# Performance work log

Hardware: AMD Instinct MI355X
Metric: run time of the kernel (lower is better)

## Reference

```python
import jax, jax.numpy as jnp
import numpy as np

B, S, H, NH, HD = 4, 2048, 2048, 16, 128
SCALE = HD ** -0.5


def rotate_half(x):
    x1, x2 = jnp.split(x, 2, axis=-1)
    return jnp.concatenate([-x2, x1], axis=-1)


def setup_inputs() -> dict:
    key = jax.random.key(0)
    ks = jax.random.split(key, 8)
    x = jax.random.normal(ks[0], (B, S, H), dtype=jnp.float32)
    # RoPE tables for positions 0..S-1, standard theta=10000 construction
    inv_freq = 1.0 / (10000.0 ** (jnp.arange(0, HD, 2, dtype=jnp.float32) / HD))
    t = jnp.arange(S, dtype=jnp.float32)
    freqs = jnp.einsum('s,d->sd', t, inv_freq)          # [S, HD/2]
    emb = jnp.concatenate([freqs, freqs], axis=-1)      # [S, HD]
    cos, sin = jnp.cos(emb), jnp.sin(emb)
    # causal mask: True = masked (future positions)
    mask = jnp.triu(jnp.ones((S, S), dtype=bool), k=1)
    std = H ** -0.5
    Wq = jax.random.normal(ks[1], (H, H), dtype=jnp.float32) * std
    Wk = jax.random.normal(ks[2], (H, H), dtype=jnp.float32) * std
    Wv = jax.random.normal(ks[3], (H, H), dtype=jnp.float32) * std
    Wo = jax.random.normal(ks[4], (H, H), dtype=jnp.float32) * std
    return {"x": x, "cos": cos, "sin": sin, "mask": mask,
            "Wq": Wq, "Wk": Wk, "Wv": Wv, "Wo": Wo}


def reference(x, cos, sin, mask, Wq, Wk, Wv, Wo):
    # projections: nn.Linear(bias=False) => x @ W.T
    def proj(W):
        y = jnp.einsum('bsh,ih->bsi', x, W)             # [B,S,inner]
        return y.reshape(B, S, NH, HD).transpose(0, 2, 1, 3)  # [B,NH,S,HD]
    q, k, v = proj(Wq), proj(Wk), proj(Wv)
    # RoPE (rotate-half), cos/sin broadcast over batch & heads
    c = cos[None, None, :, :]
    s = sin[None, None, :, :]
    q = q * c + rotate_half(q) * s
    k = k * c + rotate_half(k) * s
    # attention
    attn = jnp.einsum('bhqd,bhkd->bhqk', q, k) * SCALE
    attn = jnp.where(mask[None, None, :, :], -jnp.inf, attn)
    attn = jax.nn.softmax(attn, axis=-1)
    out = jnp.einsum('bhqk,bhkd->bhqd', attn, v)
    out = out.transpose(0, 2, 1, 3).reshape(B, S, NH * HD)
    y = jnp.einsum('bsi,hi->bsh', out, Wo)
    return y, k, v
```

## Files before the change

### kernel.cpp

```cpp
#include <hip/hip_runtime.h>
#include <hip/hip_bf16.h>
#include <math.h>

typedef __bf16 bf16_t;
typedef __bf16 bf16x8 __attribute__((ext_vector_type(8)));
typedef __bf16 bf16x4v __attribute__((ext_vector_type(4)));
typedef float  f32x4  __attribute__((ext_vector_type(4)));
typedef float  f32x16 __attribute__((ext_vector_type(16)));
typedef unsigned int u32x4 __attribute__((ext_vector_type(4)));

constexpr int CB = 4, CS = 2048, CH = 2048, CNH = 16, CHD = 128;
constexpr int CM = CB * CS;
constexpr float CSCALE = 0.08838834764831845f;
constexpr float CL2E   = 1.4426950408889634f;
constexpr float CSC2   = CSCALE * CL2E;

__device__ __forceinline__ float fexp2(float x) {
  float r;
  asm("v_exp_f32 %0, %1" : "=v"(r) : "v"(x));
  return r;
}

__device__ __forceinline__ void g2l16(const void* g, void* l) {
  __builtin_amdgcn_global_load_lds(
      (const __attribute__((address_space(1))) void*)g,
      (__attribute__((address_space(3))) void*)l, 16, 0, 0);
}

__global__ __launch_bounds__(256) void cvt_kernel(const float* __restrict__ in,
                                                  bf16_t* __restrict__ out, int n4) {
  int i = blockIdx.x * 256 + threadIdx.x;
  if (i >= n4) return;
  float4 v = reinterpret_cast<const float4*>(in)[i];
  bf16x4v o = {(bf16_t)v.x, (bf16_t)v.y, (bf16_t)v.z, (bf16_t)v.w};
  reinterpret_cast<bf16x4v*>(out)[i] = o;
}

__device__ __forceinline__ void gemm256sq_core(const bf16_t* __restrict__ A,
                                               const bf16_t* __restrict__ Bm,
                                               bf16_t (*As2)[4][64 * 64],
                                               bf16_t (*Bs2)[4][64 * 64],
                                               int row0, int col0,
                                               f32x4 (&acc)[8][4]) {
  const int tid = threadIdx.x, lane = tid & 63, w = tid >> 6;
  const int wm = w >> 2, wn = w & 3;
  constexpr int NKT = CH / 64;
  const int id = w * 64 + lane;
  const int rl = id >> 3, ck = id & 7;

  auto stA = [&](int buf, int kt, int q) {
    const int row = q * 64 + rl;
    g2l16(A + (size_t)(row0 + row) * CH + kt * 64 + ((ck ^ (row & 7)) << 3),
          &As2[buf][q][id * 8]);
  };
  auto stB = [&](int buf, int kt, int q) {
    const int row = q * 64 + rl;
    g2l16(Bm + (size_t)(col0 + row) * CH + kt * 64 + ((ck ^ (row & 7)) << 3),
          &Bs2[buf][q][id * 8]);
  };
  auto rdA = [&](int buf, int r, int c) -> bf16x8 {
    return *(const bf16x8*)(&As2[buf][r >> 6][(r & 63) * 64 + ((c ^ (r & 7)) << 3)]);
  };
  auto rdB = [&](int buf, int r, int c) -> bf16x8 {
    return *(const bf16x8*)(&Bs2[buf][r >> 6][(r & 63) * 64 + ((c ^ (r & 7)) << 3)]);
  };

#pragma unroll
  for (int q = 0; q < 4; ++q) stB(0, 0, q);
#pragma unroll
  for (int q = 0; q < 4; ++q) stA(0, 0, q);
  asm volatile("s_waitcnt vmcnt(0)" ::: "memory");
  __builtin_amdgcn_s_barrier();
  __builtin_amdgcn_sched_barrier(0);

  const int ar0 = wm * 128 + (lane & 15);
  const int br0 = wn * 64 + (lane & 15);
  const int chi = lane >> 4;

  for (int t = 0; t < NKT; ++t) {
    const int buf = t & 1, nbuf = buf ^ 1;
    const bool pf = (t + 1 < NKT);
    bf16x8 bb[4][2], aa[2][2];

#pragma unroll
    for (int p = 0; p < 4; ++p) {
      if (p == 0) {
#pragma unroll
        for (int nf = 0; nf < 4; ++nf)
#pragma unroll
          for (int kk = 0; kk < 2; ++kk)
            bb[nf][kk] = rdB(buf, br0 + nf * 16, kk * 4 + chi);
      }
#pragma unroll
      for (int i = 0; i < 2; ++i)
#pragma unroll
        for (int kk = 0; kk < 2; ++kk)
          aa[i][kk] = rdA(buf, ar0 + (2 * p + i) * 16, kk * 4 + chi);

      if (pf) {
        if (p == 0) { stB(nbuf, t + 1, 0); stB(nbuf, t + 1, 1); }
        if (p == 1) { stB(nbuf, t + 1, 2); stB(nbuf, t + 1, 3); }
        if (p == 2) { stA(nbuf, t + 1, 0); stA(nbuf, t + 1, 2); }
        if (p == 3) { stA(nbuf, t + 1, 1); stA(nbuf, t + 1, 3); }
      }

      __builtin_amdgcn_s_barrier();
      asm volatile("s_waitcnt lgkmcnt(0)" ::: "memory");
      __builtin_amdgcn_sched_barrier(0);
      __builtin_amdgcn_s_setprio(1);
#pragma unroll
      for (int i = 0; i < 2; ++i)
#pragma unroll
        for (int nf = 0; nf < 4; ++nf)
#pragma unroll
          for (int kk = 0; kk < 2; ++kk)
            acc[2 * p + i][nf] = __builtin_amdgcn_mfma_f32_16x16x32_bf16(
                aa[i][kk], bb[nf][kk], acc[2 * p + i][nf], 0, 0, 0);
      __builtin_amdgcn_s_setprio(0);

      if (p == 1) {
        if (pf) { asm volatile("s_waitcnt vmcnt(4)" ::: "memory"); }
        else    { asm volatile("s_waitcnt vmcnt(0)" ::: "memory"); }
      }
      if (p == 3 && pf) { asm volatile("s_waitcnt vmcnt(2)" ::: "memory"); }
      __builtin_amdgcn_s_barrier();
      __builtin_amdgcn_sched_barrier(0);
    }
  }
}

__global__ __launch_bounds__(512, 1) void qkv_gemm(const bf16_t* __restrict__ xb,
                                                   const bf16_t* __restrict__ wqb,
                                                   const bf16_t* __restrict__ wkb,
                                                   const bf16_t* __restrict__ wvb,
                                                   bf16_t* __restrict__ qraw,
                                                   bf16_t* __restrict__ knat,
                                                   bf16_t* __restrict__ vt2,
                                                   float* __restrict__ vout) {
  __shared__ __align__(16) bf16_t As2[2][4][64 * 64];
  __shared__ __align__(16) bf16_t Bs2[2][4][64 * 64];
  const int z = blockIdx.z;
  const bf16_t* Bm = (z == 0) ? wqb : ((z == 1) ? wkb : wvb);
  const int row0 = blockIdx.x * 256, col0 = blockIdx.y * 256;
  f32x4 acc[8][4] = {};
  gemm256sq_core(xb, Bm, As2, Bs2, row0, col0, acc);

  const int lane = threadIdx.x & 63, w = threadIdx.x >> 6;
  const int wm = w >> 2, wn = w & 3;
#pragma unroll
  for (int i = 0; i < 8; ++i) {
#pragma unroll
    for (int j = 0; j < 4; ++j) {
      const int gr0 = row0 + wm * 128 + i * 16 + (lane >> 4) * 4;
      const int gc = col0 + wn * 64 + j * 16 + (lane & 15);
      const int b = gr0 >> 11, s0 = gr0 & (CS - 1);
      const int nh = gc >> 7, hd = gc & (CHD - 1);
      const int bh = b * CNH + nh;
      if (z == 2) {
#pragma unroll
        for (int r = 0; r < 4; ++r) {
          const size_t idx = ((size_t)bh * CS + s0 + r) * CHD + hd;
          vout[idx] = acc[i][j][r];
        }
        bf16x4v pv = {(bf16_t)acc[i][j][0], (bf16_t)acc[i][j][1],
                      (bf16_t)acc[i][j][2], (bf16_t)acc[i][j][3]};
        *(bf16x4v*)(vt2 + (((size_t)bh * (CS / 16) + (s0 >> 4)) * CHD + hd) * 16 +
                    (s0 & 15)) = pv;
      } else if (z == 1) {
        bf16_t* kp = knat + (((size_t)bh * 8 + (hd >> 4)) * CS + s0) * 16 + (hd & 15);
#pragma unroll
        for (int r = 0; r < 4; ++r) kp[r * 16] = (bf16_t)acc[i][j][r];
      } else {
#pragma unroll
        for (int r = 0; r < 4; ++r) {
          const size_t idx = ((size_t)bh * CS + s0 + r) * CHD + hd;
          qraw[idx] = (bf16_t)acc[i][j][r];
        }
      }
    }
  }
}

__global__ __launch_bounds__(512, 1) void y_gemm(const bf16_t* __restrict__ ob,
                                                 const bf16_t* __restrict__ wob,
                                                 float* __restrict__ yout) {
  __shared__ __align__(16) bf16_t As2[2][4][64 * 64];
  __shared__ __align__(16) bf16_t Bs2[2][4][64 * 64];
  const int row0 = blockIdx.x * 256, col0 = blockIdx.y * 256;
  f32x4 acc[8][4] = {};
  gemm256sq_core(ob, wob, As2, Bs2, row0, col0, acc);
  const int lane = threadIdx.x & 63, w = threadIdx.x >> 6;
  const int wm = w >> 2, wn = w & 3;
#pragma unroll
  for (int i = 0; i < 8; ++i)
#pragma unroll
    for (int j = 0; j < 4; ++j)
#pragma unroll
      for (int r = 0; r < 4; ++r) {
        const int gr = row0 + wm * 128 + i * 16 + (lane >> 4) * 4 + r;
        const int gc = col0 + wn * 64 + j * 16 + (lane & 15);
        yout[(size_t)gr * CH + gc] = acc[i][j][r];
      }
}

__global__ __launch_bounds__(256) void rope_kernel(bf16_t* __restrict__ qraw,
                                                   bf16_t* __restrict__ knat,
                                                   const float* __restrict__ cosd,
                                                   const float* __restrict__ sind,
                                                   float* __restrict__ kout) {
  const int gid = blockIdx.x * 256 + threadIdx.x;
  if (blockIdx.y == 0) {
    bf16_t* p = qraw;
    const int row = gid >> 3, d0 = (gid & 7) << 3;
    const int s = row & (CS - 1);
    const size_t base = (size_t)row * CHD;
    bf16x8 v1 = *(bf16x8*)(p + base + d0);
    bf16x8 v2 = *(bf16x8*)(p + base + d0 + 64);
    float c[8], sn[8];
    *(float4*)(c)      = *(const float4*)(cosd + s * CHD + d0);
    *(float4*)(c + 4)  = *(const float4*)(cosd + s * CHD + d0 + 4);
    *(float4*)(sn)     = *(const float4*)(sind + s * CHD + d0);
    *(float4*)(sn + 4) = *(const float4*)(sind + s * CHD + d0 + 4);
    bf16x8 o1, o2;
#pragma unroll
    for (int i = 0; i < 8; ++i) {
      const float x1 = (float)v1[i], x2 = (float)v2[i];
      o1[i] = (bf16_t)(x1 * c[i] - x2 * sn[i]);
      o2[i] = (bf16_t)(x2 * c[i] + x1 * sn[i]);
    }
    *(bf16x8*)(p + base + d0) = o1;
    *(bf16x8*)(p + base + d0 + 64) = o2;
  } else {
    const int row = gid >> 3, sub = gid & 7;
    const int pan = sub >> 1, hf = (sub & 1) * 8;
    const int bh = row >> 11, s = row & (CS - 1);
    const int d0 = pan * 16 + hf;
    bf16_t* k1 = knat + (((size_t)bh * 8 + pan) * CS + s) * 16 + hf;
    bf16_t* k2 = knat + (((size_t)bh * 8 + pan + 4) * CS + s) * 16 + hf;
    bf16x8 v1 = *(bf16x8*)k1;
    bf16x8 v2 = *(bf16x8*)k2;
    float c[8], sn[8];
    *(float4*)(c)      = *(const float4*)(cosd + s * CHD + d0);
    *(float4*)(c + 4)  = *(const float4*)(cosd + s * CHD + d0 + 4);
    *(float4*)(sn)     = *(const float4*)(sind + s * CHD + d0);
    *(float4*)(sn + 4) = *(const float4*)(sind + s * CHD + d0 + 4);
    float f1[8], f2[8];
    bf16x8 o1, o2;
#pragma unroll
    for (int i = 0; i < 8; ++i) {
      const float x1 = (float)v1[i], x2 = (float)v2[i];
      f1[i] = x1 * c[i] - x2 * sn[i];
      f2[i] = x2 * c[i] + x1 * sn[i];
      o1[i] = (bf16_t)f1[i];
      o2[i] = (bf16_t)f2[i];
    }
    *(bf16x8*)k1 = o1;
    *(bf16x8*)k2 = o2;
    const size_t kb = (size_t)row * CHD + d0;
    *(float4*)(kout + kb)          = *(float4*)(f1);
    *(float4*)(kout + kb + 4)      = *(float4*)(f1 + 4);
    *(float4*)(kout + kb + 64)     = *(float4*)(f2);
    *(float4*)(kout + kb + 64 + 4) = *(float4*)(f2 + 4);
  }
}

__global__ __launch_bounds__(128) void attn_kernel(const bf16_t* __restrict__ qb,
                                                   const bf16_t* __restrict__ kn,
                                                   const bf16_t* __restrict__ v2,
                                                   bf16_t* __restrict__ ob) {
  const int tid = threadIdx.x, lane = tid & 63, w = tid >> 6;
  const int hi = lane >> 5, l31 = lane & 31;

  const int swz = (blockIdx.x & 7) * 256 + (blockIdx.x >> 3);
  const int bh = swz >> 5;
  const int qt = (31 - (swz & 31)) * 2 + w;

  const int b = bh >> 4, nh = bh & (CNH - 1);
  const bf16_t* kbase = kn + (size_t)bh * 8 * CS * 16;
  const bf16_t* vbase = v2 + (size_t)bh * (CS / 16) * CHD * 16;
  const int qw0 = qt * 32;
  const int qrow = qw0 + l31;

  bf16x8 bq[8];
  {
    const bf16_t* qp = qb + ((size_t)bh * CS + qrow) * CHD + hi * 8;
#pragma unroll
    for (int ks = 0; ks < 8; ++ks) bq[ks] = *(const bf16x8*)(qp + ks * 16);
  }

  float m_ = -INFINITY, l_ = 0.f;
  f32x16 o_[4] = {};

  const int nt = (qt >> 1) + 1;
  for (int kt = 0; kt < nt; ++kt) {
    const int kvb = kt * 64;

    f32x16 st[2] = {};
#pragma unroll
    for (int kb2 = 0; kb2 < 2; ++kb2) {
      const bf16_t* kr = kbase + (size_t)(kvb + kb2 * 32 + l31) * 16 + hi * 8;
#pragma unroll
      for (int ks = 0; ks < 8; ++ks) {
        bf16x8 ak = *(const bf16x8*)(kr + (size_t)ks * CS * 16);
        st[kb2] = __builtin_amdgcn_mfma_f32_32x32x16_bf16(ak, bq[ks], st[kb2], 0, 0, 0);
      }
    }

    const bool anymask = (kvb + 63) > qw0;
#pragma unroll
    for (int blk = 0; blk < 2; ++blk)
#pragma unroll
      for (int r = 0; r < 16; ++r) {
        float xv = st[blk][r] * CSC2;
        if (anymask) {
          const int kv = kvb + blk * 32 + 4 * hi + (r & 3) + 8 * (r >> 2);
          if (kv > qrow) xv = -INFINITY;
        }
        st[blk][r] = xv;
      }

    float tmax = st[0][0];
#pragma unroll
    for (int r = 1; r < 16; ++r) tmax = fmaxf(tmax, st[0][r]);
#pragma unroll
    for (int r = 0; r < 16; ++r) tmax = fmaxf(tmax, st[1][r]);
    tmax = fmaxf(tmax, __shfl_xor(tmax, 32, 64));

    if (__any(tmax - m_ > 8.0f)) {
      const float mn = fmaxf(m_, tmax);
      const float corr = fexp2(m_ - mn);
      m_ = mn;
      l_ *= corr;
#pragma unroll
      for (int hb = 0; hb < 4; ++hb) o_[hb] *= corr;
    }

    float psum = 0.f;
#pragma unroll
    for (int blk = 0; blk < 2; ++blk)
#pragma unroll
      for (int r = 0; r < 16; ++r) {
        const float pv = fexp2(st[blk][r] - m_);
        st[blk][r] = pv;
        psum += pv;
      }
    psum += __shfl_xor(psum, 32, 64);
    l_ += psum;

    bf16x8 pb[4];
#pragma unroll
    for (int ks = 0; ks < 4; ++ks) {
      const int blk = ks >> 1, r0 = (ks & 1) * 8;
      unsigned pw0, pw1, pw2, pw3;
      asm("v_cvt_pk_bf16_f32 %0, %1, %2" : "=v"(pw0) : "v"(st[blk][r0 + 0]), "v"(st[blk][r0 + 1]));
      asm("v_cvt_pk_bf16_f32 %0, %1, %2" : "=v"(pw2) : "v"(st[blk][r0 + 4]), "v"(st[blk][r0 + 5]));
      asm("v_cvt_pk_bf16_f32 %0, %1, %2" : "=v"(pw1) : "v"(st[blk][r0 + 2]), "v"(st[blk][r0 + 3]));
      asm("v_cvt_pk_bf16_f32 %0, %1, %2" : "=v"(pw3) : "v"(st[blk][r0 + 6]), "v"(st[blk][r0 + 7]));
      asm("v_permlane32_swap_b32 %0, %1" : "+v"(pw0), "+v"(pw2));
      asm("v_permlane32_swap_b32 %0, %1" : "+v"(pw1), "+v"(pw3));
      u32x4 pk = {pw0, pw1, pw2, pw3};
      pb[ks] = *reinterpret_cast<bf16x8*>(&pk);
    }

#pragma unroll
    for (int hb = 0; hb < 4; ++hb) {
      const bf16_t* vr = vbase + ((size_t)(kvb >> 4) * CHD + hb * 32 + l31) * 16 + hi * 8;
#pragma unroll
      for (int ks = 0; ks < 4; ++ks) {
        bf16x8 av = *(const bf16x8*)(vr + (size_t)ks * CHD * 16);
        o_[hb] = __builtin_amdgcn_mfma_f32_32x32x16_bf16(av, pb[ks], o_[hb], 0, 0, 0);
      }
    }
  }

  const float linv = 1.0f / l_;
  bf16_t* orow = ob + ((size_t)(b * CS + qrow)) * CH + nh * CHD;
#pragma unroll
  for (int hb = 0; hb < 4; ++hb)
#pragma unroll
    for (int g = 0; g < 4; ++g) {
      bf16x4v pv = {(bf16_t)(o_[hb][4 * g + 0] * linv), (bf16_t)(o_[hb][4 * g + 1] * linv),
                    (bf16_t)(o_[hb][4 * g + 2] * linv), (bf16_t)(o_[hb][4 * g + 3] * linv)};
      *(bf16x4v*)(orow + hb * 32 + 4 * hi + 8 * g) = pv;
    }
}

extern "C" void kernel_launch(void* const* d_in, const int* in_sizes, int n_in,
                              void* d_out, int out_size, void* d_ws, size_t ws_size,
                              hipStream_t stream) {
  const float* x    = (const float*)d_in[0];
  const float* cosd = (const float*)d_in[1];
  const float* sind = (const float*)d_in[2];
  const float* Wq = (const float*)d_in[4];
  const float* Wk = (const float*)d_in[5];
  const float* Wv = (const float*)d_in[6];
  const float* Wo = (const float*)d_in[7];

  float* yout = (float*)d_out;
  float* kout = yout + (size_t)CM * CH;
  float* vout = kout + (size_t)CM * CH;

  char* ws = (char*)d_ws;
  size_t off = 0;
  auto wsalloc = [&](size_t bytes) {
    void* p = ws + off;
    off += (bytes + 255) & ~(size_t)255;
    return p;
  };
  bf16_t* xb   = (bf16_t*)wsalloc((size_t)CM * CH * 2);
  bf16_t* wqb  = (bf16_t*)wsalloc((size_t)CH * CH * 2);
  bf16_t* wkb  = (bf16_t*)wsalloc((size_t)CH * CH * 2);
  bf16_t* wvb  = (bf16_t*)wsalloc((size_t)CH * CH * 2);
  bf16_t* wob  = (bf16_t*)wsalloc((size_t)CH * CH * 2);
  bf16_t* qraw = (bf16_t*)wsalloc((size_t)CM * CH * 2);
  bf16_t* knat = (bf16_t*)wsalloc((size_t)CM * CH * 2);
  bf16_t* vt2  = (bf16_t*)wsalloc((size_t)CM * CH * 2);
  bf16_t* ob   = (bf16_t*)wsalloc((size_t)CM * CH * 2);

  cvt_kernel<<<CM * CH / 4 / 256, 256, 0, stream>>>(x, xb, CM * CH / 4);
  cvt_kernel<<<CH * CH / 4 / 256, 256, 0, stream>>>(Wq, wqb, CH * CH / 4);
  cvt_kernel<<<CH * CH / 4 / 256, 256, 0, stream>>>(Wk, wkb, CH * CH / 4);
  cvt_kernel<<<CH * CH / 4 / 256, 256, 0, stream>>>(Wv, wvb, CH * CH / 4);
  cvt_kernel<<<CH * CH / 4 / 256, 256, 0, stream>>>(Wo, wob, CH * CH / 4);

  qkv_gemm<<<dim3(CM / 256, CH / 256, 3), 512, 0, stream>>>(xb, wqb, wkb, wvb,
                                                            qraw, knat, vt2, vout);
  rope_kernel<<<dim3(CB * CNH * CS * 8 / 256, 2), 256, 0, stream>>>(qraw, knat, cosd,
                                                                    sind, kout);
  attn_kernel<<<CB * CNH * (CS / 64), 128, 0, stream>>>(qraw, knat, vt2, ob);
  y_gemm<<<dim3(CM / 256, CH / 256), 512, 0, stream>>>(ob, wob, yout);
}
```

Before: 532.3 us.

## Split attention KV loop across two waves per query tile with LDS merge

Each block now handles one 32-row query tile, and its two waves process alternating KV tiles. The second wave writes its partial O, max and sum to shared memory, and the first wave merges them with rescaling before writing the output. Twice as many blocks are launched, which is meant to improve load balance and occupancy across the causal triangle. The cost is an extra LDS round trip, a barrier, and Q loads that are duplicated per wave.

```diff
diff --git a/kernel.cpp b/kernel.cpp
--- a/kernel.cpp
+++ b/kernel.cpp
@@ -268,12 +268,14 @@
                                                    const bf16_t* __restrict__ kn,
                                                    const bf16_t* __restrict__ v2,
                                                    bf16_t* __restrict__ ob) {
-  const int tid = threadIdx.x, lane = tid & 63, w = tid >> 6;
+  __shared__ float Os[32][129];
+  __shared__ float Ms[32], Ls[32];
+  const int tid = threadIdx.x, lane = tid & 63, wh = tid >> 6;
   const int hi = lane >> 5, l31 = lane & 31;
 
-  const int swz = (blockIdx.x & 7) * 256 + (blockIdx.x >> 3);
-  const int bh = swz >> 5;
-  const int qt = (31 - (swz & 31)) * 2 + w;
+  const int swz = (blockIdx.x & 7) * 512 + (blockIdx.x >> 3);
+  const int bh = swz >> 6;
+  const int qt = 63 - (swz & 63);
 
   const int b = bh >> 4, nh = bh & (CNH - 1);
   const bf16_t* kbase = kn + (size_t)bh * 8 * CS * 16;
@@ -292,7 +294,7 @@
   f32x16 o_[4] = {};
 
   const int nt = (qt >> 1) + 1;
-  for (int kt = 0; kt < nt; ++kt) {
+  for (int kt = wh; kt < nt; kt += 2) {
     const int kvb = kt * 64;
 
     f32x16 st[2] = {};
@@ -373,15 +375,35 @@
     }
   }
 
-  const float linv = 1.0f / l_;
+  if (wh == 1) {
+#pragma unroll
+    for (int hb = 0; hb < 4; ++hb)
+#pragma unroll
+      for (int r = 0; r < 16; ++r) {
+        const int hd = 32 * hb + 4 * hi + (r & 3) + 8 * (r >> 2);
+        Os[l31][hd] = o_[hb][r];
+      }
+    if (hi == 0) { Ms[l31] = m_; Ls[l31] = l_; }
+  }
+  __builtin_amdgcn_s_barrier();
+  if (wh == 1) return;
+
+  const float m1 = Ms[l31], l1 = Ls[l31];
+  const float mn = fmaxf(m_, m1);
+  const float c0 = fexp2(m_ - mn), c1 = fexp2(m1 - mn);
+  const float linv = 1.0f / (l_ * c0 + l1 * c1);
   bf16_t* orow = ob + ((size_t)(b * CS + qrow)) * CH + nh * CHD;
 #pragma unroll
   for (int hb = 0; hb < 4; ++hb)
 #pragma unroll
     for (int g = 0; g < 4; ++g) {
-      bf16x4v pv = {(bf16_t)(o_[hb][4 * g + 0] * linv), (bf16_t)(o_[hb][4 * g + 1] * linv),
-                    (bf16_t)(o_[hb][4 * g + 2] * linv), (bf16_t)(o_[hb][4 * g + 3] * linv)};
-      *(bf16x4v*)(orow + hb * 32 + 4 * hi + 8 * g) = pv;
+      const int hd0 = 32 * hb + 4 * hi + 8 * g;
+      bf16x4v pv = {
+          (bf16_t)((o_[hb][4 * g + 0] * c0 + Os[l31][hd0 + 0] * c1) * linv),
+          (bf16_t)((o_[hb][4 * g + 1] * c0 + Os[l31][hd0 + 1] * c1) * linv),
+          (bf16_t)((o_[hb][4 * g + 2] * c0 + Os[l31][hd0 + 2] * c1) * linv),
+          (bf16_t)((o_[hb][4 * g + 3] * c0 + Os[l31][hd0 + 3] * c1) * linv)};
+      *(bf16x4v*)(orow + hd0) = pv;
     }
 }
 
@@ -427,6 +449,6 @@
                                                             qraw, knat, vt2, vout);
   rope_kernel<<<dim3(CB * CNH * CS * 8 / 256, 2), 256, 0, stream>>>(qraw, knat, cosd,
                                                                     sind, kout);
-  attn_kernel<<<CB * CNH * (CS / 64), 128, 0, stream>>>(qraw, knat, vt2, ob);
+  attn_kernel<<<CB * CNH * (CS / 32), 128, 0, stream>>>(qraw, knat, vt2, ob);
   y_gemm<<<dim3(CM / 256, CH / 256), 512, 0, stream>>>(ob, wob, yout);
 }
```

New measurement: 518.0 us. 1.03x faster.
